# Kernel optimization log

Hardware: AMD Instinct MI355X
Metric: run time of the kernel (lower is better)

The kernel has to match this reference:

```python
import jax, jax.numpy as jnp
import numpy as np

N = 6144      # total nodes = num_data_qubits + num_checks
NQ = 3072     # num_data_qubits
D = 128       # hidden_dim
H = 4         # attention heads
C = D // H    # per-head channels (GATConv out_channels)
F_IN = 10     # node_feature_dim
L = 4         # num_gnn_layers
E = 393216    # num edges (before self-loops)


def _ln(x, g, b):
    m = x.mean(-1, keepdims=True)
    v = ((x - m) ** 2).mean(-1, keepdims=True)
    return (x - m) / jnp.sqrt(v + 1e-5) * g + b


def setup_inputs() -> dict:
    key = jax.random.key(0)
    ks = iter(jax.random.split(key, 64))

    def nrm(shape, scale):
        return jax.random.normal(next(ks), shape, jnp.float32) * scale

    inp = {}
    inp["node_features"] = nrm((N, F_IN), 1.0)
    inp["edge_index"] = jax.random.randint(next(ks), (2, E), 0, N, jnp.int32)
    inp["partner_encoding"] = nrm((N, D), 1.0)
    # node embedding MLP
    inp["emb_W"] = nrm((F_IN, D), F_IN ** -0.5)
    inp["emb_b"] = jnp.zeros((D,), jnp.float32)
    inp["emb_ln_g"] = jnp.ones((D,), jnp.float32)
    inp["emb_ln_b"] = jnp.zeros((D,), jnp.float32)
    # GAT layers (stacked over L)
    inp["gat_W"] = nrm((L, D, D), D ** -0.5)
    inp["gat_a_src"] = nrm((L, H, C), C ** -0.5)
    inp["gat_a_dst"] = nrm((L, H, C), C ** -0.5)
    inp["gat_b"] = jnp.zeros((L, D), jnp.float32)
    inp["ln_g"] = jnp.ones((L, D), jnp.float32)
    inp["ln_b"] = jnp.zeros((L, D), jnp.float32)
    # cross-panel multihead attention
    for nm in ["Wq", "Wk", "Wv", "Wo"]:
        inp[nm] = nrm((D, D), D ** -0.5)
    for nm in ["bq", "bk", "bv", "bo"]:
        inp[nm] = jnp.zeros((D,), jnp.float32)
    inp["ca_ln_g"] = jnp.ones((D,), jnp.float32)
    inp["ca_ln_b"] = jnp.zeros((D,), jnp.float32)
    # policy head
    inp["pW1"] = nrm((D, D), D ** -0.5); inp["pb1"] = jnp.zeros((D,), jnp.float32)
    inp["pW2"] = nrm((D, D // 2), D ** -0.5); inp["pb2"] = jnp.zeros((D // 2,), jnp.float32)
    inp["pW3"] = nrm((D // 2, 2), (D // 2) ** -0.5); inp["pb3"] = jnp.zeros((2,), jnp.float32)
    # value head
    inp["vW1"] = nrm((D, D), D ** -0.5); inp["vb1"] = jnp.zeros((D,), jnp.float32)
    inp["vW2"] = nrm((D, D // 2), D ** -0.5); inp["vb2"] = jnp.zeros((D // 2,), jnp.float32)
    inp["vW3"] = nrm((D // 2, 1), (D // 2) ** -0.5); inp["vb3"] = jnp.zeros((1,), jnp.float32)
    return inp


def reference(node_features, edge_index, partner_encoding,
              emb_W, emb_b, emb_ln_g, emb_ln_b,
              gat_W, gat_a_src, gat_a_dst, gat_b, ln_g, ln_b,
              Wq, bq, Wk, bk, Wv, bv, Wo, bo, ca_ln_g, ca_ln_b,
              pW1, pb1, pW2, pb2, pW3, pb3,
              vW1, vb1, vW2, vb2, vW3, vb3):
    # PyG GATConv default: add self-loops
    loops = jnp.arange(N, dtype=edge_index.dtype)
    src = jnp.concatenate([edge_index[0], loops])  # message source j
    dst = jnp.concatenate([edge_index[1], loops])  # aggregation target i

    x = jax.nn.relu(_ln(node_features @ emb_W + emb_b, emb_ln_g, emb_ln_b))

    for l in range(L):
        h = (x @ gat_W[l]).reshape(N, H, C)
        a_s = (h * gat_a_src[l]).sum(-1)  # [N,H]
        a_d = (h * gat_a_dst[l]).sum(-1)  # [N,H]
        e = jax.nn.leaky_relu(a_s[src] + a_d[dst], 0.2)  # [E+N,H]
        # segment softmax over edges sharing destination node
        mx = jax.ops.segment_max(e, dst, num_segments=N)
        ex = jnp.exp(e - mx[dst])
        denom = jax.ops.segment_sum(ex, dst, num_segments=N)
        alpha = ex / (denom[dst] + 1e-16)
        out = jax.ops.segment_sum(alpha[:, :, None] * h[src], dst, num_segments=N)
        out = out.reshape(N, D) + gat_b[l]
        x = _ln(x + jax.nn.relu(out), ln_g[l], ln_b[l])

    # cross-panel multihead attention (eval mode, batch of 1)
    q = (x @ Wq + bq).reshape(N, H, C)
    k = (partner_encoding @ Wk + bk).reshape(N, H, C)
    v = (partner_encoding @ Wv + bv).reshape(N, H, C)
    att = jax.nn.softmax(jnp.einsum('nhd,mhd->hnm', q, k) / np.float32(np.sqrt(C)), axis=-1)
    xa = jnp.einsum('hnm,mhd->nhd', att, v).reshape(N, D) @ Wo + bo
    x = _ln(x + xa, ca_ln_g, ca_ln_b)

    dq = x[:NQ]
    logits = jax.nn.relu(jax.nn.relu(dq @ pW1 + pb1) @ pW2 + pb2) @ pW3 + pb3
    pooled = x.mean(0, keepdims=True)
    value = jax.nn.relu(jax.nn.relu(pooled @ vW1 + vb1) @ vW2 + vb2) @ vW3 + vb3
    return logits, value, x
```

## Files before the change

### kernel.cpp

```cpp
#include <hip/hip_runtime.h>
#include <hip/hip_bf16.h>

#define N_NODES 6144
#define NQ_ 3072
#define D 128
#define H 4
#define C 32
#define F_IN 10
#define L_LAYERS 4
#define E_EDGES 393216
#define E_TOT (E_EDGES + N_NODES)
#define SPLITS 8
#define KV_PER (N_NODES / SPLITS)
#define NT_TOT (N_NODES / 32)
#define LOG2E 1.4426950408889634f

typedef __attribute__((ext_vector_type(8))) short bf16x8;
typedef __attribute__((ext_vector_type(4))) float f32x4;
typedef __attribute__((ext_vector_type(16))) float f32x16;

__device__ __forceinline__ unsigned short f2bf(float f) {
  unsigned u = __float_as_uint(f);
  unsigned r = (u + 0x7fffu + ((u >> 16) & 1u)) >> 16;
  return (unsigned short)r;
}

__device__ __forceinline__ float bf2f(unsigned short s) {
  return __uint_as_float(((unsigned)s) << 16);
}

__device__ __forceinline__ unsigned cvtpk(float lo, float hi) {
  unsigned r;
  asm volatile("v_cvt_pk_bf16_f32 %0, %1, %2" : "=v"(r) : "v"(lo), "v"(hi));
  return r;
}

#define P32SWAP(a, b) asm volatile("v_permlane32_swap_b32 %0, %1" : "+v"(a), "+v"(b))

__device__ __forceinline__ float red128_sum(float v, float* tmp2, int tid) {
#pragma unroll
  for (int m = 1; m < 64; m <<= 1) v += __shfl_xor(v, m, 64);
  __syncthreads();
  if ((tid & 63) == 0) tmp2[tid >> 6] = v;
  __syncthreads();
  return tmp2[0] + tmp2[1];
}

__global__ void k_zero(int* cnt, int* cur, float* pooled) {
  int i = blockIdx.x * blockDim.x + threadIdx.x;
  if (i < N_NODES) { cnt[i] = 0; cur[i] = 0; }
  if (i < D) pooled[i] = 0.f;
}

__global__ void k_hist(const int* __restrict__ dst, int* __restrict__ cnt) {
  for (int i = blockIdx.x * blockDim.x + threadIdx.x; i < E_EDGES; i += gridDim.x * blockDim.x)
    atomicAdd(&cnt[dst[i]], 1);
}

__global__ void k_scan(const int* __restrict__ cnt, int* __restrict__ indptr) {
  __shared__ int ps[256];
  int tid = threadIdx.x;
  const int CH = N_NODES / 256;
  int base = tid * CH;
  int loc[CH];
  int s = 0;
#pragma unroll
  for (int i = 0; i < CH; i++) { loc[i] = cnt[base + i] + 1; s += loc[i]; }
  ps[tid] = s;
  __syncthreads();
  for (int off = 1; off < 256; off <<= 1) {
    int v = (tid >= off) ? ps[tid - off] : 0;
    __syncthreads();
    ps[tid] += v;
    __syncthreads();
  }
  int run = (tid == 0) ? 0 : ps[tid - 1];
#pragma unroll
  for (int i = 0; i < CH; i++) { indptr[base + i] = run; run += loc[i]; }
  if (tid == 255) indptr[N_NODES] = run;
}

__global__ void k_scatter(const int* __restrict__ src, const int* __restrict__ dst,
                          const int* __restrict__ indptr, int* __restrict__ cur,
                          int* __restrict__ sorted) {
  for (int i = blockIdx.x * blockDim.x + threadIdx.x; i < E_TOT; i += gridDim.x * blockDim.x) {
    if (i < E_EDGES) {
      int d = dst[i];
      int p = atomicAdd(&cur[d], 1);
      sorted[indptr[d] + p] = src[i];
    } else {
      int n = i - E_EDGES;
      int p = atomicAdd(&cur[n], 1);
      sorted[indptr[n] + p] = n;
    }
  }
}

__global__ __launch_bounds__(128) void k_embed(const float* __restrict__ nf,
                                               const float* __restrict__ W,
                                               const float* __restrict__ b,
                                               const float* __restrict__ g,
                                               const float* __restrict__ bb,
                                               float* __restrict__ x,
                                               unsigned short* __restrict__ xbf) {
  int n = blockIdx.x, j = threadIdx.x;
  __shared__ float f[F_IN];
  __shared__ float tmp2[2];
  if (j < F_IN) f[j] = nf[n * F_IN + j];
  __syncthreads();
  float acc = b[j];
#pragma unroll
  for (int k = 0; k < F_IN; k++) acc += f[k] * W[k * D + j];
  float s1 = red128_sum(acc, tmp2, j);
  float s2 = red128_sum(acc * acc, tmp2, j);
  float mean = s1 * (1.f / D);
  float var = s2 * (1.f / D) - mean * mean;
  float y = (acc - mean) * rsqrtf(var + 1e-5f) * g[j] + bb[j];
  y = fmaxf(y, 0.f);
  x[n * D + j] = y;
  xbf[n * D + j] = f2bf(y);
}

__global__ void k_wprep(const float* __restrict__ W, unsigned short* __restrict__ wt) {
  int i = blockIdx.x * 256 + threadIdx.x;
  int l = i >> 14, rem = i & 16383, j = rem >> 7, k = rem & 127;
  wt[i] = f2bf(W[l * 16384 + k * 128 + j]);
}

#define MFMA32(A, B, CIN) __builtin_amdgcn_mfma_f32_32x32x16_bf16(A, B, CIN, 0, 0, 0)

__global__ __launch_bounds__(256) void k_gat_gemm(const unsigned short* __restrict__ xbf,
                                                  const unsigned short* __restrict__ wt,
                                                  unsigned short* __restrict__ hbf) {
  int t = threadIdx.x;
  int w = t >> 6, l = t & 63, qc = l & 31, hi = l >> 5;
  int tile = blockIdx.x * 4 + w;
  int row0 = (tile >> 2) * 32, col0 = (tile & 3) * 32;
  const unsigned short* ap = xbf + (size_t)(row0 + qc) * D + hi * 8;
  const unsigned short* bp = wt + (size_t)(col0 + qc) * D + hi * 8;
  f32x16 o = {0.f};
#pragma unroll
  for (int kk = 0; kk < 8; kk++) {
    bf16x8 a = *(const bf16x8*)(ap + kk * 16);
    bf16x8 b = *(const bf16x8*)(bp + kk * 16);
    o = MFMA32(a, b, o);
  }
#pragma unroll
  for (int r = 0; r < 16; r++) {
    int rr = (r & 3) + 8 * (r >> 2) + 4 * hi;
    hbf[(size_t)(row0 + rr) * D + col0 + qc] = f2bf(o[r]);
  }
}

__global__ __launch_bounds__(128) void k_gat_attn(const unsigned short* __restrict__ hbf,
                                                  const float* __restrict__ asrc,
                                                  const float* __restrict__ adst,
                                                  float* __restrict__ a_s,
                                                  float* __restrict__ a_d) {
  int t = threadIdx.x;
  int ni = t >> 4, j = t & 15;
  int n = blockIdx.x * 8 + ni;
  const unsigned short* hp = hbf + (size_t)n * D + j * 8;
  float p = 0.f, q = 0.f;
#pragma unroll
  for (int c = 0; c < 8; c++) {
    float hv = bf2f(hp[c]);
    p += hv * asrc[j * 8 + c];
    q += hv * adst[j * 8 + c];
  }
  p += __shfl_xor(p, 1); p += __shfl_xor(p, 2);
  q += __shfl_xor(q, 1); q += __shfl_xor(q, 2);
  if ((j & 3) == 0) {
    int head = j >> 2;
    a_s[n * H + head] = p * LOG2E;
    a_d[n * H + head] = q * LOG2E;
  }
}

__device__ __forceinline__ float leaky(float v) { return v > 0.f ? v : 0.2f * v; }

__global__ __launch_bounds__(128) void k_gat_agg(const unsigned short* __restrict__ hbf,
                                                 const float* __restrict__ a_s,
                                                 const float* __restrict__ a_d,
                                                 const int* __restrict__ indptr,
                                                 const int* __restrict__ sorted,
                                                 const float* __restrict__ gb,
                                                 const float* __restrict__ g,
                                                 const float* __restrict__ bb,
                                                 float* __restrict__ x,
                                                 unsigned short* __restrict__ xbf) {
  int n = blockIdx.x, tid = threadIdx.x;
  int beg = indptr[n], end = indptr[n + 1];
  __shared__ int s_src[128];
  __shared__ float s_ex[128 * 4];
  __shared__ float tmp2[2];
  float4 ad = *(const float4*)&a_d[n * H];
  int hd = tid >> 5;
  float acc = 0.f;
  float d0 = 0.f, d1 = 0.f, d2 = 0.f, d3 = 0.f;

  for (int c0 = beg; c0 < end; c0 += 128) {
    __syncthreads();
    int e = c0 + tid;
    if (e < end) {
      int s = sorted[e];
      s_src[tid] = s;
      float4 as = *(const float4*)&a_s[s * H];
      float e0 = exp2f(leaky(as.x + ad.x));
      float e1 = exp2f(leaky(as.y + ad.y));
      float e2 = exp2f(leaky(as.z + ad.z));
      float e3 = exp2f(leaky(as.w + ad.w));
      s_ex[tid * 4 + 0] = e0;
      s_ex[tid * 4 + 1] = e1;
      s_ex[tid * 4 + 2] = e2;
      s_ex[tid * 4 + 3] = e3;
      d0 += e0; d1 += e1; d2 += e2; d3 += e3;
    }
    __syncthreads();
    int nc = min(128, end - c0);
#pragma unroll 4
    for (int i = 0; i < nc; i++) {
      acc += s_ex[i * 4 + hd] * bf2f(hbf[s_src[i] * D + tid]);
    }
  }
  float t0 = red128_sum(d0, tmp2, tid);
  float t1 = red128_sum(d1, tmp2, tid);
  float t2 = red128_sum(d2, tmp2, tid);
  float t3 = red128_sum(d3, tmp2, tid);
  float dd = (hd == 0) ? t0 : (hd == 1) ? t1 : (hd == 2) ? t2 : t3;
  float out = acc * (1.f / (dd + 1e-16f)) + gb[tid];
  float y = x[n * D + tid] + fmaxf(out, 0.f);
  float s1 = red128_sum(y, tmp2, tid);
  float s2 = red128_sum(y * y, tmp2, tid);
  float mean = s1 * (1.f / D);
  float var = s2 * (1.f / D) - mean * mean;
  float o = (y - mean) * rsqrtf(var + 1e-5f) * g[tid] + bb[tid];
  x[n * D + tid] = o;
  xbf[n * D + tid] = f2bf(o);
}

__global__ __launch_bounds__(128) void k_qkv(const float* __restrict__ x,
                                             const float* __restrict__ pe,
                                             const float* __restrict__ Wq,
                                             const float* __restrict__ Wk,
                                             const float* __restrict__ Wv,
                                             const float* __restrict__ bq,
                                             const float* __restrict__ bk,
                                             const float* __restrict__ bv,
                                             unsigned short* __restrict__ qbf,
                                             unsigned short* __restrict__ kpk,
                                             unsigned short* __restrict__ vpk) {
  int tid = threadIdx.x, r0 = blockIdx.x * 8;
  __shared__ float xs[8][D], ps[8][D];
#pragma unroll
  for (int r = 0; r < 8; r++) {
    xs[r][tid] = x[(r0 + r) * D + tid];
    ps[r][tid] = pe[(r0 + r) * D + tid];
  }
  __syncthreads();
  float aq[8], ak[8], av[8];
#pragma unroll
  for (int r = 0; r < 8; r++) { aq[r] = 0.f; ak[r] = 0.f; av[r] = 0.f; }
  for (int kk = 0; kk < D; kk++) {
    float wq = Wq[kk * D + tid], wk = Wk[kk * D + tid], wv = Wv[kk * D + tid];
#pragma unroll
    for (int r = 0; r < 8; r++) {
      aq[r] += xs[r][kk] * wq;
      ak[r] += ps[r][kk] * wk;
      av[r] += ps[r][kk] * wv;
    }
  }
  const float sc = 0.25503491f;
  float bqv = bq[tid], bkv = bk[tid], bvv = bv[tid];
  int hh = tid >> 5, cw = tid & 31;
  int kfrag = (cw >> 4) & 1, khi = (cw >> 3) & 1, kj = cw & 7;
#pragma unroll
  for (int r = 0; r < 8; r++) {
    int n = r0 + r;
    int kt = n >> 5, qn = n & 31;
    qbf[(size_t)n * D + tid] = f2bf((aq[r] + bqv) * sc);
    kpk[((((size_t)hh * NT_TOT + kt) * 2 + kfrag) * 64 + khi * 32 + qn) * 8 + kj] = f2bf(ak[r] + bkv);
    int vfrag = (qn >> 4) & 1, vhi = (qn >> 3) & 1, vj = qn & 7;
    vpk[((((size_t)hh * NT_TOT + kt) * 2 + vfrag) * 64 + vhi * 32 + cw) * 8 + vj] = f2bf(av[r] + bvv);
  }
}

#define ALOAD(KA0, KA1, VB0_, VB1_, TI) do { \
  const unsigned short* kp_ = kB + (size_t)(TI) * 1024 + l8; \
  const unsigned short* vp_ = vB + (size_t)(TI) * 1024 + l8; \
  KA0 = *(const bf16x8*)(kp_); \
  KA1 = *(const bf16x8*)(kp_ + 512); \
  VB0_ = *(const bf16x8*)(vp_); \
  VB1_ = *(const bf16x8*)(vp_ + 512); \
} while (0)

#define TILE32(KA0, KA1, VB0_, VB1_, O, LS) do { \
  f32x16 s = MFMA32(KA0, qa0, zz16); \
  s = MFMA32(KA1, qa1, s); \
  float p0 = __builtin_amdgcn_exp2f(s[0]), p1 = __builtin_amdgcn_exp2f(s[1]); \
  float p2 = __builtin_amdgcn_exp2f(s[2]), p3 = __builtin_amdgcn_exp2f(s[3]); \
  float p4 = __builtin_amdgcn_exp2f(s[4]), p5 = __builtin_amdgcn_exp2f(s[5]); \
  float p6 = __builtin_amdgcn_exp2f(s[6]), p7 = __builtin_amdgcn_exp2f(s[7]); \
  float p8 = __builtin_amdgcn_exp2f(s[8]), p9 = __builtin_amdgcn_exp2f(s[9]); \
  float pa = __builtin_amdgcn_exp2f(s[10]), pc = __builtin_amdgcn_exp2f(s[11]); \
  float pd = __builtin_amdgcn_exp2f(s[12]), pe_ = __builtin_amdgcn_exp2f(s[13]); \
  float pf = __builtin_amdgcn_exp2f(s[14]), pg = __builtin_amdgcn_exp2f(s[15]); \
  LS += (((p0 + p1) + (p2 + p3)) + ((p4 + p5) + (p6 + p7))) + \
        (((p8 + p9) + (pa + pc)) + ((pd + pe_) + (pf + pg))); \
  unsigned x0_ = cvtpk(p0, p1), x1_ = cvtpk(p2, p3); \
  unsigned y0_ = cvtpk(p4, p5), y1_ = cvtpk(p6, p7); \
  P32SWAP(x0_, y0_); P32SWAP(x1_, y1_); \
  unsigned x2_ = cvtpk(p8, p9), x3_ = cvtpk(pa, pc); \
  unsigned y2_ = cvtpk(pd, pe_), y3_ = cvtpk(pf, pg); \
  P32SWAP(x2_, y2_); P32SWAP(x3_, y3_); \
  union { unsigned u[4]; bf16x8 v; } fa_, fb_; \
  fa_.u[0] = x0_; fa_.u[1] = x1_; fa_.u[2] = y0_; fa_.u[3] = y1_; \
  fb_.u[0] = x2_; fb_.u[1] = x3_; fb_.u[2] = y2_; fb_.u[3] = y3_; \
  O = MFMA32(VB0_, fa_.v, O); \
  O = MFMA32(VB1_, fb_.v, O); \
} while (0)

__global__ __launch_bounds__(256) void k_attn_split(const unsigned short* __restrict__ qbf,
                                                    const unsigned short* __restrict__ kpk,
                                                    const unsigned short* __restrict__ vpk,
                                                    unsigned short* __restrict__ po,
                                                    float* __restrict__ pl) {
  int hh = blockIdx.y;
  int sp = blockIdx.z;
  int t = threadIdx.x;
  int wid = t >> 6, l = t & 63;
  int qc = l & 31, hi = l >> 5;
  int l8 = l * 8;
  int q0w = blockIdx.x * 128 + wid * 32;

  const f32x16 zz16 = {0.f};

  const unsigned short* qp = qbf + (size_t)(q0w + qc) * D + hh * 32 + hi * 8;
  bf16x8 qa0 = *(const bf16x8*)(qp);
  bf16x8 qa1 = *(const bf16x8*)(qp + 16);

  const unsigned short* kB = kpk + ((size_t)hh * NT_TOT + sp * (KV_PER / 32)) * 1024;
  const unsigned short* vB = vpk + ((size_t)hh * NT_TOT + sp * (KV_PER / 32)) * 1024;

  f32x16 oA = {0.f}, oB = {0.f};
  float lsA = 0.f, lsB = 0.f;

  bf16x8 ka0, ka1, va0, va1, kb0r, kb1r, vb0r, vb1r;
  ALOAD(ka0, ka1, va0, va1, 0);
  const int NT = KV_PER / 32;
  for (int it = 0; it < NT; it += 2) {
    ALOAD(kb0r, kb1r, vb0r, vb1r, it + 1);
    TILE32(ka0, ka1, va0, va1, oA, lsA);
    if (it + 2 < NT) ALOAD(ka0, ka1, va0, va1, it + 2);
    TILE32(kb0r, kb1r, vb0r, vb1r, oB, lsB);
  }

  f32x16 o = oA + oB;
  float lsum = lsA + lsB;
  float lt = lsum + __shfl_xor(lsum, 32, 64);
  size_t pbase = (size_t)(sp * H + hh) * N_NODES + q0w + qc;
  unsigned short* pop = po + pbase * 32 + 4 * hi;
  uint2 v0, v1, v2, v3;
  v0.x = cvtpk(o[0], o[1]);   v0.y = cvtpk(o[2], o[3]);
  v1.x = cvtpk(o[4], o[5]);   v1.y = cvtpk(o[6], o[7]);
  v2.x = cvtpk(o[8], o[9]);   v2.y = cvtpk(o[10], o[11]);
  v3.x = cvtpk(o[12], o[13]); v3.y = cvtpk(o[14], o[15]);
  *(uint2*)(pop)      = v0;
  *(uint2*)(pop + 8)  = v1;
  *(uint2*)(pop + 16) = v2;
  *(uint2*)(pop + 24) = v3;
  if (l < 32) {
    pl[pbase] = lt;
  }
}

__global__ __launch_bounds__(256) void k_attn_combine(const unsigned short* __restrict__ po,
                                                      const float* __restrict__ pl,
                                                      float* __restrict__ xa) {
  int t = blockIdx.x * 256 + threadIdx.x;
  int q = t >> 6, cp = t & 63;
  int c2 = cp * 2, hh = c2 >> 5, c = c2 & 31;
  int base = hh * N_NODES + q;
  const int SN = H * N_NODES;
  float ll = 0.f, olo = 0.f, ohi = 0.f;
#pragma unroll
  for (int s = 0; s < SPLITS; s++) {
    ll += pl[s * SN + base];
    unsigned dw = *(const unsigned*)(po + ((size_t)(s * SN + base)) * 32 + c);
    olo += bf2f((unsigned short)(dw & 0xffff));
    ohi += bf2f((unsigned short)(dw >> 16));
  }
  float inv = 1.f / ll;
  float* op = xa + (size_t)q * D + hh * 32 + c;
  op[0] = olo * inv;
  op[1] = ohi * inv;
}

__global__ __launch_bounds__(128) void k_ca(const float* __restrict__ xa,
                                            const float* __restrict__ Wo,
                                            const float* __restrict__ bo,
                                            const float* __restrict__ g,
                                            const float* __restrict__ bb,
                                            float* __restrict__ x, float* __restrict__ pooled,
                                            float* __restrict__ outx) {
  int tid = threadIdx.x, r0 = blockIdx.x * 8;
  __shared__ float xs[8][D];
  __shared__ float tmp2[2];
#pragma unroll
  for (int r = 0; r < 8; r++) xs[r][tid] = xa[(r0 + r) * D + tid];
  __syncthreads();
  float acc[8];
#pragma unroll
  for (int r = 0; r < 8; r++) acc[r] = bo[tid];
  for (int kk = 0; kk < D; kk++) {
    float w = Wo[kk * D + tid];
#pragma unroll
    for (int r = 0; r < 8; r++) acc[r] += xs[r][kk] * w;
  }
  float gv = g[tid], bv = bb[tid];
  float psum = 0.f;
#pragma unroll
  for (int r = 0; r < 8; r++) {
    float y = x[(r0 + r) * D + tid] + acc[r];
    float t1 = red128_sum(y, tmp2, tid);
    float t2 = red128_sum(y * y, tmp2, tid);
    float mean = t1 * (1.f / D);
    float var = t2 * (1.f / D) - mean * mean;
    float o = (y - mean) * rsqrtf(var + 1e-5f) * gv + bv;
    x[(r0 + r) * D + tid] = o;
    outx[(r0 + r) * D + tid] = o;
    psum += o;
  }
  atomicAdd(&pooled[tid], psum);
}

__global__ __launch_bounds__(128) void k_policy(const float* __restrict__ x,
                                                const float* __restrict__ W1,
                                                const float* __restrict__ b1,
                                                const float* __restrict__ W2,
                                                const float* __restrict__ b2,
                                                const float* __restrict__ W3,
                                                const float* __restrict__ b3,
                                                float* __restrict__ logits) {
  int n = blockIdx.x, tid = threadIdx.x;
  __shared__ float xs[D], h1[D], h2[64];
  xs[tid] = x[n * D + tid];
  __syncthreads();
  float a = b1[tid];
  for (int kk = 0; kk < D; kk++) a += xs[kk] * W1[kk * D + tid];
  h1[tid] = fmaxf(a, 0.f);
  __syncthreads();
  if (tid < 64) {
    float a2 = b2[tid];
    for (int kk = 0; kk < D; kk++) a2 += h1[kk] * W2[kk * 64 + tid];
    h2[tid] = fmaxf(a2, 0.f);
  }
  __syncthreads();
  float p0 = 0.f, p1 = 0.f;
  if (tid < 64) { p0 = h2[tid] * W3[tid * 2]; p1 = h2[tid] * W3[tid * 2 + 1]; }
#pragma unroll
  for (int m = 1; m < 64; m <<= 1) { p0 += __shfl_xor(p0, m, 64); p1 += __shfl_xor(p1, m, 64); }
  if (tid == 0) {
    logits[n * 2] = p0 + b3[0];
    logits[n * 2 + 1] = p1 + b3[1];
  }
}

__global__ __launch_bounds__(128) void k_value(const float* __restrict__ pooled,
                                               const float* __restrict__ W1,
                                               const float* __restrict__ b1,
                                               const float* __restrict__ W2,
                                               const float* __restrict__ b2,
                                               const float* __restrict__ W3,
                                               const float* __restrict__ b3,
                                               float* __restrict__ val) {
  int tid = threadIdx.x;
  __shared__ float ps[D], v1[D], v2[64];
  ps[tid] = pooled[tid] * (1.f / N_NODES);
  __syncthreads();
  float a = b1[tid];
  for (int kk = 0; kk < D; kk++) a += ps[kk] * W1[kk * D + tid];
  v1[tid] = fmaxf(a, 0.f);
  __syncthreads();
  if (tid < 64) {
    float a2 = b2[tid];
    for (int kk = 0; kk < D; kk++) a2 += v1[kk] * W2[kk * 64 + tid];
    v2[tid] = fmaxf(a2, 0.f);
  }
  __syncthreads();
  float p = (tid < 64) ? v2[tid] * W3[tid] : 0.f;
#pragma unroll
  for (int m = 1; m < 64; m <<= 1) p += __shfl_xor(p, m, 64);
  if (tid == 0) val[0] = p + b3[0];
}

extern "C" void kernel_launch(void* const* d_in, const int* in_sizes, int n_in,
                              void* d_out, int out_size, void* d_ws, size_t ws_size,
                              hipStream_t stream) {
  const float* nf   = (const float*)d_in[0];
  const int*   ei   = (const int*)d_in[1];
  const float* pe   = (const float*)d_in[2];
  const float* embW = (const float*)d_in[3];
  const float* embB = (const float*)d_in[4];
  const float* elng = (const float*)d_in[5];
  const float* elnb = (const float*)d_in[6];
  const float* gatW = (const float*)d_in[7];
  const float* aS   = (const float*)d_in[8];
  const float* aD   = (const float*)d_in[9];
  const float* gatB = (const float*)d_in[10];
  const float* lng  = (const float*)d_in[11];
  const float* lnb  = (const float*)d_in[12];
  const float* Wq   = (const float*)d_in[13];
  const float* Wk   = (const float*)d_in[14];
  const float* Wv   = (const float*)d_in[15];
  const float* Wo   = (const float*)d_in[16];
  const float* bq   = (const float*)d_in[17];
  const float* bk   = (const float*)d_in[18];
  const float* bv   = (const float*)d_in[19];
  const float* bo   = (const float*)d_in[20];
  const float* cag  = (const float*)d_in[21];
  const float* cab  = (const float*)d_in[22];
  const float* pW1  = (const float*)d_in[23];
  const float* pb1  = (const float*)d_in[24];
  const float* pW2  = (const float*)d_in[25];
  const float* pb2  = (const float*)d_in[26];
  const float* pW3  = (const float*)d_in[27];
  const float* pb3  = (const float*)d_in[28];
  const float* vW1  = (const float*)d_in[29];
  const float* vb1  = (const float*)d_in[30];
  const float* vW2  = (const float*)d_in[31];
  const float* vb2  = (const float*)d_in[32];
  const float* vW3  = (const float*)d_in[33];
  const float* vb3  = (const float*)d_in[34];

  float* fw = (float*)d_ws;
  float* x      = fw; fw += N_NODES * D;
  float* hbuf   = fw; fw += N_NODES * D;
  float* a_s    = fw; fw += N_NODES * H;
  float* a_d    = fw; fw += N_NODES * H;
  float* pooled = fw; fw += 128;
  float* pl     = fw; fw += SPLITS * H * N_NODES;
  unsigned short* ub = (unsigned short*)fw;
  unsigned short* po  = ub; ub += (size_t)SPLITS * H * N_NODES * 32;
  unsigned short* qbf = ub; ub += N_NODES * D;
  unsigned short* kpk = ub; ub += N_NODES * D;
  unsigned short* vpk = ub; ub += N_NODES * D;
  unsigned short* xbf = ub; ub += N_NODES * D;
  unsigned short* wtb = ub; ub += L_LAYERS * D * D;
  int* ib     = (int*)ub;
  int* cnt    = ib; ib += N_NODES;
  int* cur    = ib; ib += N_NODES;
  int* indptr = ib; ib += N_NODES + 16;
  int* sorted = ib;

  unsigned short* hbf = (unsigned short*)hbuf;

  float* out    = (float*)d_out;
  float* logits = out;
  float* val    = out + NQ_ * 2;
  float* outx   = out + NQ_ * 2 + 1;

  const int* esrc = ei;
  const int* edst = ei + E_EDGES;

  hipLaunchKernelGGL(k_zero, dim3(24), dim3(256), 0, stream, cnt, cur, pooled);
  hipLaunchKernelGGL(k_hist, dim3(512), dim3(256), 0, stream, edst, cnt);
  hipLaunchKernelGGL(k_scan, dim3(1), dim3(256), 0, stream, cnt, indptr);
  hipLaunchKernelGGL(k_scatter, dim3(512), dim3(256), 0, stream, esrc, edst, indptr, cur, sorted);
  hipLaunchKernelGGL(k_embed, dim3(N_NODES), dim3(128), 0, stream, nf, embW, embB, elng, elnb, x, xbf);
  hipLaunchKernelGGL(k_wprep, dim3(L_LAYERS * D * D / 256), dim3(256), 0, stream, gatW, wtb);
  for (int l = 0; l < L_LAYERS; l++) {
    hipLaunchKernelGGL(k_gat_gemm, dim3(N_NODES / 32), dim3(256), 0, stream,
                       xbf, wtb + l * D * D, hbf);
    hipLaunchKernelGGL(k_gat_attn, dim3(N_NODES / 8), dim3(128), 0, stream,
                       hbf, aS + l * D, aD + l * D, a_s, a_d);
    hipLaunchKernelGGL(k_gat_agg, dim3(N_NODES), dim3(128), 0, stream,
                       hbf, a_s, a_d, indptr, sorted, gatB + l * D, lng + l * D, lnb + l * D, x, xbf);
  }
  hipLaunchKernelGGL(k_qkv, dim3(N_NODES / 8), dim3(128), 0, stream,
                     x, pe, Wq, Wk, Wv, bq, bk, bv, qbf, kpk, vpk);
  hipLaunchKernelGGL(k_attn_split, dim3(N_NODES / 128, H, SPLITS), dim3(256), 0, stream,
                     qbf, kpk, vpk, po, pl);
  hipLaunchKernelGGL(k_attn_combine, dim3(N_NODES * D / 512), dim3(256), 0, stream,
                     po, pl, hbuf);
  hipLaunchKernelGGL(k_ca, dim3(N_NODES / 8), dim3(128), 0, stream,
                     hbuf, Wo, bo, cag, cab, x, pooled, outx);
  hipLaunchKernelGGL(k_policy, dim3(NQ_), dim3(128), 0, stream,
                     x, pW1, pb1, pW2, pb2, pW3, pb3, logits);
  hipLaunchKernelGGL(k_value, dim3(1), dim3(128), 0, stream,
                     pooled, vW1, vb1, vW2, vb2, vW3, vb3, val);
}
```

Baseline: 306.6 us.

## Move QKV, output projection and policy MLP GEMMs onto bf16 MFMA

Replaces the scalar FP32 GEMMs for the Q/K/V projections, the cross-attention output projection and the policy MLP with bf16 32x32x16 MFMA tile kernels sharing a helper. Weights and the partner encoding are pre-converted and transposed to bf16, and the attention combine now writes bf16. The fused k_ca kernel becomes a GEMM plus a separate LayerNorm pass, and the policy head becomes three kernels. This removes slow FP32 FMA loops at the cost of extra launches, extra bf16 rounding and extra intermediate traffic.

```diff
diff --git a/kernel.cpp b/kernel.cpp
--- a/kernel.cpp
+++ b/kernel.cpp
@@ -37,6 +37,8 @@
 
 #define P32SWAP(a, b) asm volatile("v_permlane32_swap_b32 %0, %1" : "+v"(a), "+v"(b))
 
+#define MFMA32(A, B, CIN) __builtin_amdgcn_mfma_f32_32x32x16_bf16(A, B, CIN, 0, 0, 0)
+
 __device__ __forceinline__ float red128_sum(float v, float* tmp2, int tid) {
 #pragma unroll
   for (int m = 1; m < 64; m <<= 1) v += __shfl_xor(v, m, 64);
@@ -44,6 +46,21 @@
   if ((tid & 63) == 0) tmp2[tid >> 6] = v;
   __syncthreads();
   return tmp2[0] + tmp2[1];
+}
+
+__device__ __forceinline__ f32x16 tile_gemm128(const unsigned short* __restrict__ A,
+                                               const unsigned short* __restrict__ Bt,
+                                               int row0, int col0, int qc, int hi) {
+  const unsigned short* ap = A + (size_t)(row0 + qc) * 128 + hi * 8;
+  const unsigned short* bp = Bt + (size_t)(col0 + qc) * 128 + hi * 8;
+  f32x16 o = {0.f};
+#pragma unroll
+  for (int kk = 0; kk < 8; kk++) {
+    bf16x8 a = *(const bf16x8*)(ap + kk * 16);
+    bf16x8 b = *(const bf16x8*)(bp + kk * 16);
+    o = MFMA32(a, b, o);
+  }
+  return o;
 }
 
 __global__ void k_zero(int* cnt, int* cur, float* pooled) {
@@ -127,7 +144,34 @@
   wt[i] = f2bf(W[l * 16384 + k * 128 + j]);
 }
 
-#define MFMA32(A, B, CIN) __builtin_amdgcn_mfma_f32_32x32x16_bf16(A, B, CIN, 0, 0, 0)
+__global__ void k_wqkvprep(const float* __restrict__ Wq, const float* __restrict__ Wk,
+                           const float* __restrict__ Wv, const float* __restrict__ W1,
+                           const float* __restrict__ W2, const float* __restrict__ Wo,
+                           unsigned short* __restrict__ wqt, unsigned short* __restrict__ wkt,
+                           unsigned short* __restrict__ wvt, unsigned short* __restrict__ w1t,
+                           unsigned short* __restrict__ w2t, unsigned short* __restrict__ wot) {
+  int i = blockIdx.x * 256 + threadIdx.x;
+  if (i < 65536) {
+    int m = i >> 14, loc = i & 16383, j = loc >> 7, k = loc & 127;
+    const float* src = (m == 0) ? Wq : (m == 1) ? Wk : (m == 2) ? Wv : W1;
+    unsigned short* dst = (m == 0) ? wqt : (m == 1) ? wkt : (m == 2) ? wvt : w1t;
+    dst[loc] = f2bf(src[k * 128 + j]);
+  } else if (i < 73728) {
+    int loc = i - 65536, j = loc >> 7, k = loc & 127;
+    w2t[loc] = f2bf(W2[k * 64 + j]);
+  } else if (i < 90112) {
+    int loc = i - 73728, j = loc >> 7, k = loc & 127;
+    wot[loc] = f2bf(Wo[k * 128 + j]);
+  }
+}
+
+__global__ void k_pebf(const float* __restrict__ pe, unsigned short* __restrict__ pebf) {
+  int i = blockIdx.x * 256 + threadIdx.x;
+  float4 v = *(const float4*)(pe + (size_t)i * 4);
+  unsigned lo = (unsigned)f2bf(v.x) | ((unsigned)f2bf(v.y) << 16);
+  unsigned hi = (unsigned)f2bf(v.z) | ((unsigned)f2bf(v.w) << 16);
+  *(uint2*)(pebf + (size_t)i * 4) = make_uint2(lo, hi);
+}
 
 __global__ __launch_bounds__(256) void k_gat_gemm(const unsigned short* __restrict__ xbf,
                                                   const unsigned short* __restrict__ wt,
@@ -136,15 +180,7 @@
   int w = t >> 6, l = t & 63, qc = l & 31, hi = l >> 5;
   int tile = blockIdx.x * 4 + w;
   int row0 = (tile >> 2) * 32, col0 = (tile & 3) * 32;
-  const unsigned short* ap = xbf + (size_t)(row0 + qc) * D + hi * 8;
-  const unsigned short* bp = wt + (size_t)(col0 + qc) * D + hi * 8;
-  f32x16 o = {0.f};
-#pragma unroll
-  for (int kk = 0; kk < 8; kk++) {
-    bf16x8 a = *(const bf16x8*)(ap + kk * 16);
-    bf16x8 b = *(const bf16x8*)(bp + kk * 16);
-    o = MFMA32(a, b, o);
-  }
+  f32x16 o = tile_gemm128(xbf, wt, row0, col0, qc, hi);
 #pragma unroll
   for (int r = 0; r < 16; r++) {
     int rr = (r & 3) + 8 * (r >> 2) + 4 * hi;
@@ -239,49 +275,53 @@
   xbf[n * D + tid] = f2bf(o);
 }
 
-__global__ __launch_bounds__(128) void k_qkv(const float* __restrict__ x,
-                                             const float* __restrict__ pe,
-                                             const float* __restrict__ Wq,
-                                             const float* __restrict__ Wk,
-                                             const float* __restrict__ Wv,
-                                             const float* __restrict__ bq,
-                                             const float* __restrict__ bk,
-                                             const float* __restrict__ bv,
-                                             unsigned short* __restrict__ qbf,
-                                             unsigned short* __restrict__ kpk,
-                                             unsigned short* __restrict__ vpk) {
-  int tid = threadIdx.x, r0 = blockIdx.x * 8;
-  __shared__ float xs[8][D], ps[8][D];
-#pragma unroll
-  for (int r = 0; r < 8; r++) {
-    xs[r][tid] = x[(r0 + r) * D + tid];
-    ps[r][tid] = pe[(r0 + r) * D + tid];
-  }
-  __syncthreads();
-  float aq[8], ak[8], av[8];
-#pragma unroll
-  for (int r = 0; r < 8; r++) { aq[r] = 0.f; ak[r] = 0.f; av[r] = 0.f; }
-  for (int kk = 0; kk < D; kk++) {
-    float wq = Wq[kk * D + tid], wk = Wk[kk * D + tid], wv = Wv[kk * D + tid];
-#pragma unroll
-    for (int r = 0; r < 8; r++) {
-      aq[r] += xs[r][kk] * wq;
-      ak[r] += ps[r][kk] * wk;
-      av[r] += ps[r][kk] * wv;
+__global__ __launch_bounds__(256) void k_qkv_mfma(const unsigned short* __restrict__ xbf,
+                                                  const unsigned short* __restrict__ pebf,
+                                                  const unsigned short* __restrict__ wqt,
+                                                  const unsigned short* __restrict__ wkt,
+                                                  const unsigned short* __restrict__ wvt,
+                                                  const float* __restrict__ bq,
+                                                  const float* __restrict__ bk,
+                                                  const float* __restrict__ bv,
+                                                  unsigned short* __restrict__ qbf,
+                                                  unsigned short* __restrict__ kpk,
+                                                  unsigned short* __restrict__ vpk) {
+  int t = threadIdx.x;
+  int w = t >> 6, l = t & 63, qc = l & 31, hi = l >> 5;
+  int m = blockIdx.y;
+  int row0 = blockIdx.x * 32, col0 = w * 32;
+  const unsigned short* A = (m == 0) ? xbf : pebf;
+  const unsigned short* Bt = (m == 0) ? wqt : (m == 1) ? wkt : wvt;
+  f32x16 o = tile_gemm128(A, Bt, row0, col0, qc, hi);
+  int c = col0 + qc;
+  int hh = col0 >> 5;
+  int kt = row0 >> 5;
+  if (m == 0) {
+    const float sc = 0.25503491f;
+    float bias = bq[c];
+#pragma unroll
+    for (int r = 0; r < 16; r++) {
+      int rr = (r & 3) + 8 * (r >> 2) + 4 * hi;
+      qbf[(size_t)(row0 + rr) * D + c] = f2bf((o[r] + bias) * sc);
     }
-  }
-  const float sc = 0.25503491f;
-  float bqv = bq[tid], bkv = bk[tid], bvv = bv[tid];
-  int hh = tid >> 5, cw = tid & 31;
-  int kfrag = (cw >> 4) & 1, khi = (cw >> 3) & 1, kj = cw & 7;
-#pragma unroll
-  for (int r = 0; r < 8; r++) {
-    int n = r0 + r;
-    int kt = n >> 5, qn = n & 31;
-    qbf[(size_t)n * D + tid] = f2bf((aq[r] + bqv) * sc);
-    kpk[((((size_t)hh * NT_TOT + kt) * 2 + kfrag) * 64 + khi * 32 + qn) * 8 + kj] = f2bf(ak[r] + bkv);
-    int vfrag = (qn >> 4) & 1, vhi = (qn >> 3) & 1, vj = qn & 7;
-    vpk[((((size_t)hh * NT_TOT + kt) * 2 + vfrag) * 64 + vhi * 32 + cw) * 8 + vj] = f2bf(av[r] + bvv);
+  } else if (m == 1) {
+    float bias = bk[c];
+    int kfrag = (qc >> 4) & 1, khi = (qc >> 3) & 1, kj = qc & 7;
+    unsigned short* base = kpk + ((((size_t)hh * NT_TOT + kt) * 2 + kfrag) * 64 + khi * 32) * 8 + kj;
+#pragma unroll
+    for (int r = 0; r < 16; r++) {
+      int rr = (r & 3) + 8 * (r >> 2) + 4 * hi;
+      base[rr * 8] = f2bf(o[r] + bias);
+    }
+  } else {
+    float bias = bv[c];
+#pragma unroll
+    for (int r = 0; r < 16; r++) {
+      int rr = (r & 3) + 8 * (r >> 2) + 4 * hi;
+      int vfrag = (rr >> 4) & 1, vhi = (rr >> 3) & 1, vj = rr & 7;
+      vpk[((((size_t)hh * NT_TOT + kt) * 2 + vfrag) * 64 + vhi * 32 + qc) * 8 + vj] =
+          f2bf(o[r] + bias);
+    }
   }
 }
 
@@ -376,7 +416,7 @@
 
 __global__ __launch_bounds__(256) void k_attn_combine(const unsigned short* __restrict__ po,
                                                       const float* __restrict__ pl,
-                                                      float* __restrict__ xa) {
+                                                      unsigned short* __restrict__ xabf) {
   int t = blockIdx.x * 256 + threadIdx.x;
   int q = t >> 6, cp = t & 63;
   int c2 = cp * 2, hh = c2 >> 5, c = c2 & 31;
@@ -391,76 +431,98 @@
     ohi += bf2f((unsigned short)(dw >> 16));
   }
   float inv = 1.f / ll;
-  float* op = xa + (size_t)q * D + hh * 32 + c;
-  op[0] = olo * inv;
-  op[1] = ohi * inv;
-}
-
-__global__ __launch_bounds__(128) void k_ca(const float* __restrict__ xa,
-                                            const float* __restrict__ Wo,
-                                            const float* __restrict__ bo,
-                                            const float* __restrict__ g,
-                                            const float* __restrict__ bb,
-                                            float* __restrict__ x, float* __restrict__ pooled,
-                                            float* __restrict__ outx) {
+  *(unsigned*)(xabf + (size_t)q * D + c2) = cvtpk(olo * inv, ohi * inv);
+}
+
+__global__ __launch_bounds__(256) void k_ca_gemm(const unsigned short* __restrict__ xabf,
+                                                 const unsigned short* __restrict__ wot,
+                                                 const float* __restrict__ bo,
+                                                 float* __restrict__ yb) {
+  int t = threadIdx.x;
+  int w = t >> 6, l = t & 63, qc = l & 31, hi = l >> 5;
+  int row0 = blockIdx.x * 32, col0 = w * 32;
+  f32x16 o = tile_gemm128(xabf, wot, row0, col0, qc, hi);
+  float bias = bo[col0 + qc];
+#pragma unroll
+  for (int r = 0; r < 16; r++) {
+    int rr = (r & 3) + 8 * (r >> 2) + 4 * hi;
+    yb[(size_t)(row0 + rr) * D + col0 + qc] = o[r] + bias;
+  }
+}
+
+__global__ __launch_bounds__(128) void k_ca_ln(const float* __restrict__ yb,
+                                               const float* __restrict__ g,
+                                               const float* __restrict__ bb,
+                                               float* __restrict__ x,
+                                               unsigned short* __restrict__ xbf,
+                                               float* __restrict__ pooled,
+                                               float* __restrict__ outx) {
   int tid = threadIdx.x, r0 = blockIdx.x * 8;
-  __shared__ float xs[8][D];
   __shared__ float tmp2[2];
-#pragma unroll
-  for (int r = 0; r < 8; r++) xs[r][tid] = xa[(r0 + r) * D + tid];
-  __syncthreads();
-  float acc[8];
-#pragma unroll
-  for (int r = 0; r < 8; r++) acc[r] = bo[tid];
-  for (int kk = 0; kk < D; kk++) {
-    float w = Wo[kk * D + tid];
-#pragma unroll
-    for (int r = 0; r < 8; r++) acc[r] += xs[r][kk] * w;
-  }
   float gv = g[tid], bv = bb[tid];
   float psum = 0.f;
 #pragma unroll
   for (int r = 0; r < 8; r++) {
-    float y = x[(r0 + r) * D + tid] + acc[r];
+    int n = r0 + r;
+    float y = x[n * D + tid] + yb[n * D + tid];
     float t1 = red128_sum(y, tmp2, tid);
     float t2 = red128_sum(y * y, tmp2, tid);
     float mean = t1 * (1.f / D);
     float var = t2 * (1.f / D) - mean * mean;
     float o = (y - mean) * rsqrtf(var + 1e-5f) * gv + bv;
-    x[(r0 + r) * D + tid] = o;
-    outx[(r0 + r) * D + tid] = o;
+    x[n * D + tid] = o;
+    xbf[n * D + tid] = f2bf(o);
+    outx[n * D + tid] = o;
     psum += o;
   }
   atomicAdd(&pooled[tid], psum);
 }
 
-__global__ __launch_bounds__(128) void k_policy(const float* __restrict__ x,
-                                                const float* __restrict__ W1,
-                                                const float* __restrict__ b1,
-                                                const float* __restrict__ W2,
-                                                const float* __restrict__ b2,
-                                                const float* __restrict__ W3,
-                                                const float* __restrict__ b3,
-                                                float* __restrict__ logits) {
-  int n = blockIdx.x, tid = threadIdx.x;
-  __shared__ float xs[D], h1[D], h2[64];
-  xs[tid] = x[n * D + tid];
-  __syncthreads();
-  float a = b1[tid];
-  for (int kk = 0; kk < D; kk++) a += xs[kk] * W1[kk * D + tid];
-  h1[tid] = fmaxf(a, 0.f);
-  __syncthreads();
-  if (tid < 64) {
-    float a2 = b2[tid];
-    for (int kk = 0; kk < D; kk++) a2 += h1[kk] * W2[kk * 64 + tid];
-    h2[tid] = fmaxf(a2, 0.f);
-  }
-  __syncthreads();
-  float p0 = 0.f, p1 = 0.f;
-  if (tid < 64) { p0 = h2[tid] * W3[tid * 2]; p1 = h2[tid] * W3[tid * 2 + 1]; }
+__global__ __launch_bounds__(256) void k_policy1(const unsigned short* __restrict__ xbf,
+                                                 const unsigned short* __restrict__ w1t,
+                                                 const float* __restrict__ b1,
+                                                 unsigned short* __restrict__ h1) {
+  int t = threadIdx.x;
+  int w = t >> 6, l = t & 63, qc = l & 31, hi = l >> 5;
+  int row0 = blockIdx.x * 32, col0 = w * 32;
+  f32x16 o = tile_gemm128(xbf, w1t, row0, col0, qc, hi);
+  float bias = b1[col0 + qc];
+#pragma unroll
+  for (int r = 0; r < 16; r++) {
+    int rr = (r & 3) + 8 * (r >> 2) + 4 * hi;
+    h1[(size_t)(row0 + rr) * D + col0 + qc] = f2bf(fmaxf(o[r] + bias, 0.f));
+  }
+}
+
+__global__ __launch_bounds__(128) void k_policy2(const unsigned short* __restrict__ h1,
+                                                 const unsigned short* __restrict__ w2t,
+                                                 const float* __restrict__ b2,
+                                                 unsigned short* __restrict__ h2) {
+  int t = threadIdx.x;
+  int w = t >> 6, l = t & 63, qc = l & 31, hi = l >> 5;
+  int row0 = blockIdx.x * 32, col0 = w * 32;
+  f32x16 o = tile_gemm128(h1, w2t, row0, col0, qc, hi);
+  float bias = b2[col0 + qc];
+#pragma unroll
+  for (int r = 0; r < 16; r++) {
+    int rr = (r & 3) + 8 * (r >> 2) + 4 * hi;
+    h2[(size_t)(row0 + rr) * 64 + col0 + qc] = f2bf(fmaxf(o[r] + bias, 0.f));
+  }
+}
+
+__global__ __launch_bounds__(256) void k_policy3(const unsigned short* __restrict__ h2,
+                                                 const float* __restrict__ W3,
+                                                 const float* __restrict__ b3,
+                                                 float* __restrict__ logits) {
+  int t = threadIdx.x;
+  int wv = t >> 6, l = t & 63;
+  int n = blockIdx.x * 4 + wv;
+  float h = bf2f(h2[(size_t)n * 64 + l]);
+  float p0 = h * W3[l * 2];
+  float p1 = h * W3[l * 2 + 1];
 #pragma unroll
   for (int m = 1; m < 64; m <<= 1) { p0 += __shfl_xor(p0, m, 64); p1 += __shfl_xor(p1, m, 64); }
-  if (tid == 0) {
+  if (l == 0) {
     logits[n * 2] = p0 + b3[0];
     logits[n * 2 + 1] = p1 + b3[1];
   }
@@ -541,19 +603,30 @@
   float* pooled = fw; fw += 128;
   float* pl     = fw; fw += SPLITS * H * N_NODES;
   unsigned short* ub = (unsigned short*)fw;
-  unsigned short* po  = ub; ub += (size_t)SPLITS * H * N_NODES * 32;
-  unsigned short* qbf = ub; ub += N_NODES * D;
-  unsigned short* kpk = ub; ub += N_NODES * D;
-  unsigned short* vpk = ub; ub += N_NODES * D;
-  unsigned short* xbf = ub; ub += N_NODES * D;
-  unsigned short* wtb = ub; ub += L_LAYERS * D * D;
+  unsigned short* po   = ub; ub += (size_t)SPLITS * H * N_NODES * 32;
+  unsigned short* qbf  = ub; ub += N_NODES * D;
+  unsigned short* kpk  = ub; ub += N_NODES * D;
+  unsigned short* vpk  = ub; ub += N_NODES * D;
+  unsigned short* xbf  = ub; ub += N_NODES * D;
+  unsigned short* pebf = ub; ub += N_NODES * D;
+  unsigned short* wtb  = ub; ub += L_LAYERS * D * D;
+  unsigned short* wqt  = ub; ub += D * D;
+  unsigned short* wkt  = ub; ub += D * D;
+  unsigned short* wvt  = ub; ub += D * D;
+  unsigned short* w1t  = ub; ub += D * D;
+  unsigned short* w2t  = ub; ub += 64 * D;
+  unsigned short* wot  = ub; ub += D * D;
   int* ib     = (int*)ub;
   int* cnt    = ib; ib += N_NODES;
   int* cur    = ib; ib += N_NODES;
   int* indptr = ib; ib += N_NODES + 16;
   int* sorted = ib;
 
-  unsigned short* hbf = (unsigned short*)hbuf;
+  unsigned short* hbf  = (unsigned short*)hbuf;
+  float* yb            = hbuf;
+  unsigned short* xabf = kpk;
+  unsigned short* h1   = qbf;
+  unsigned short* h2   = qbf + (size_t)NQ_ * D;
 
   float* out    = (float*)d_out;
   float* logits = out;
@@ -569,6 +642,9 @@
   hipLaunchKernelGGL(k_scatter, dim3(512), dim3(256), 0, stream, esrc, edst, indptr, cur, sorted);
   hipLaunchKernelGGL(k_embed, dim3(N_NODES), dim3(128), 0, stream, nf, embW, embB, elng, elnb, x, xbf);
   hipLaunchKernelGGL(k_wprep, dim3(L_LAYERS * D * D / 256), dim3(256), 0, stream, gatW, wtb);
+  hipLaunchKernelGGL(k_wqkvprep, dim3(352), dim3(256), 0, stream,
+                     Wq, Wk, Wv, pW1, pW2, Wo, wqt, wkt, wvt, w1t, w2t, wot);
+  hipLaunchKernelGGL(k_pebf, dim3(N_NODES * D / 1024), dim3(256), 0, stream, pe, pebf);
   for (int l = 0; l < L_LAYERS; l++) {
     hipLaunchKernelGGL(k_gat_gemm, dim3(N_NODES / 32), dim3(256), 0, stream,
                        xbf, wtb + l * D * D, hbf);
@@ -577,16 +653,18 @@
     hipLaunchKernelGGL(k_gat_agg, dim3(N_NODES), dim3(128), 0, stream,
                        hbf, a_s, a_d, indptr, sorted, gatB + l * D, lng + l * D, lnb + l * D, x, xbf);
   }
-  hipLaunchKernelGGL(k_qkv, dim3(N_NODES / 8), dim3(128), 0, stream,
-                     x, pe, Wq, Wk, Wv, bq, bk, bv, qbf, kpk, vpk);
+  hipLaunchKernelGGL(k_qkv_mfma, dim3(N_NODES / 32, 3), dim3(256), 0, stream,
+                     xbf, pebf, wqt, wkt, wvt, bq, bk, bv, qbf, kpk, vpk);
   hipLaunchKernelGGL(k_attn_split, dim3(N_NODES / 128, H, SPLITS), dim3(256), 0, stream,
                      qbf, kpk, vpk, po, pl);
   hipLaunchKernelGGL(k_attn_combine, dim3(N_NODES * D / 512), dim3(256), 0, stream,
-                     po, pl, hbuf);
-  hipLaunchKernelGGL(k_ca, dim3(N_NODES / 8), dim3(128), 0, stream,
-                     hbuf, Wo, bo, cag, cab, x, pooled, outx);
-  hipLaunchKernelGGL(k_policy, dim3(NQ_), dim3(128), 0, stream,
-                     x, pW1, pb1, pW2, pb2, pW3, pb3, logits);
+                     po, pl, xabf);
+  hipLaunchKernelGGL(k_ca_gemm, dim3(N_NODES / 32), dim3(256), 0, stream, xabf, wot, bo, yb);
+  hipLaunchKernelGGL(k_ca_ln, dim3(N_NODES / 8), dim3(128), 0, stream,
+                     yb, cag, cab, x, xbf, pooled, outx);
+  hipLaunchKernelGGL(k_policy1, dim3(NQ_ / 32), dim3(256), 0, stream, xbf, w1t, pb1, h1);
+  hipLaunchKernelGGL(k_policy2, dim3(NQ_ / 32), dim3(128), 0, stream, h1, w2t, pb2, h2);
+  hipLaunchKernelGGL(k_policy3, dim3(NQ_ / 4), dim3(256), 0, stream, h2, pW3, pb3, logits);
   hipLaunchKernelGGL(k_value, dim3(1), dim3(128), 0, stream,
                      pooled, vW1, vb1, vW2, vb2, vW3, vb3, val);
 }
```

Result: faster. 273.9 us (-10.7%).
